# Optimization experiments

Hardware: AMD Instinct MI355X
Metric: run time of the kernel (lower is better)

The kernel has to match this reference:

```python
import jax, jax.numpy as jnp
import numpy as np

N_HEAD = 32


def _apply_rope(x, rope):
    # x: (B, H, T, hs); rope: (block_size, hs//2) angles
    B, H, T, hs = x.shape
    ang = rope[:T]  # (T, hs//2)
    cos = jnp.cos(ang)[None, :, None, :]  # (1, T, 1, hs//2)
    sin = jnp.sin(ang)[None, :, None, :]
    xt = x.transpose(0, 2, 1, 3).reshape(B, T, H, hs // 2, 2)
    x0, x1 = xt[..., 0], xt[..., 1]
    out_r = x0 * cos - x1 * sin
    out_i = x0 * sin + x1 * cos
    out = jnp.stack([out_r, out_i], axis=-1).reshape(B, T, H, hs)
    return out.transpose(0, 2, 1, 3)


def setup_inputs() -> dict:
    key = jax.random.key(0)
    ks = jax.random.split(key, 6)
    B, T, C = 2, 2048, 4096
    aT = 10
    hs = C // N_HEAD
    return {
        "x": jax.random.normal(ks[0], (B, T, C), dtype=jnp.float32),
        "adaption_prompt": jax.random.normal(ks[1], (1, aT, C), dtype=jnp.float32),
        "rope_cache": jax.random.uniform(ks[2], (4096, hs // 2), dtype=jnp.float32) * 2.0 * np.pi,
        "w_attn": jax.random.normal(ks[3], (C, 3 * C), dtype=jnp.float32) * 0.02,
        "w_proj": jax.random.normal(ks[4], (C, C), dtype=jnp.float32) * 0.02,
        "gating_factor": jax.random.normal(ks[5], (1,), dtype=jnp.float32) * 0.1,
    }


def reference(x, adaption_prompt, rope_cache, w_attn, w_proj, gating_factor):
    B, T, C = x.shape
    H = N_HEAD
    hs = C // H

    qkv = x @ w_attn  # (B, T, 3C)
    q, k, v = jnp.split(qkv, 3, axis=2)
    q = q.reshape(B, T, H, hs).transpose(0, 2, 1, 3)  # (B, H, T, hs)
    k = k.reshape(B, T, H, hs).transpose(0, 2, 1, 3)
    v = v.reshape(B, T, H, hs).transpose(0, 2, 1, 3)

    q = _apply_rope(q, rope_cache)
    k = _apply_rope(k, rope_cache)

    # causal SDPA, scale = 1/sqrt(head_size)
    scale = 1.0 / jnp.sqrt(jnp.asarray(hs, dtype=q.dtype))
    scores = jnp.einsum("bhqd,bhkd->bhqk", q, k) * scale
    causal = jnp.tril(jnp.ones((T, T), dtype=bool))
    scores = jnp.where(causal[None, None, :, :], scores, jnp.asarray(-jnp.inf, scores.dtype))
    attn = jax.nn.softmax(scores, axis=-1)
    y = jnp.einsum("bhqk,bhkd->bhqd", attn, v)  # (B, H, T, hs)

    # adapter attention (note: scale uses full n_embd, as in source)
    aT = adaption_prompt.shape[1]
    aqkv = adaption_prompt @ w_attn  # (1, aT, 3C)
    _, ak, av = jnp.split(aqkv, 3, axis=2)
    ak = ak.reshape(1, aT, H, hs).transpose(0, 2, 1, 3)  # (1, H, aT, hs)
    av = av.reshape(1, aT, H, hs).transpose(0, 2, 1, 3)
    ascores = jnp.einsum("bhqd,xhkd->bhqk", q, ak) / jnp.sqrt(jnp.asarray(C, q.dtype))
    ascores = gating_factor[0] * jax.nn.softmax(ascores.astype(jnp.float32), axis=-1).astype(q.dtype)
    y = y + jnp.einsum("bhqk,xhkd->bhqd", ascores, av)

    y = y.transpose(0, 2, 1, 3).reshape(B, T, C)
    return y @ w_proj
```

## Files before the change

kernel.cpp:

```cpp
#include <hip/hip_runtime.h>

typedef unsigned short u16;
typedef unsigned int u32;
typedef __attribute__((ext_vector_type(4))) float f32x4;
typedef __attribute__((ext_vector_type(8))) _Float16 half8;
typedef __attribute__((ext_vector_type(8))) unsigned short u16x8;
typedef __attribute__((ext_vector_type(4))) unsigned short u16x4;

static __device__ __forceinline__ u16 f2h(float f) {
  union { _Float16 h; u16 u; } c;
  c.h = (_Float16)f;
  return c.u;
}
static __device__ __forceinline__ float h2f(u16 u) {
  union { _Float16 h; u16 u; } c;
  c.u = u;
  return (float)c.h;
}
static __device__ __forceinline__ void gload_lds16(const void* g, void* l) {
  __builtin_amdgcn_global_load_lds((const __attribute__((address_space(1))) void*)g,
                                   (__attribute__((address_space(3))) void*)l,
                                   16, 0, 0);
}

__global__ __launch_bounds__(256) void transpose_cvt(const float* __restrict__ src,
                                                     u16* __restrict__ dst,
                                                     int R, int C) {
  __shared__ float tile[32][33];
  const int tx = threadIdx.x, ty = threadIdx.y;
  const int c0 = blockIdx.x << 5, r0 = blockIdx.y << 5;
#pragma unroll
  for (int i = 0; i < 32; i += 8)
    tile[ty + i][tx] = src[(size_t)(r0 + ty + i) * C + c0 + tx];
  __syncthreads();
#pragma unroll
  for (int i = 0; i < 32; i += 8)
    dst[(size_t)(c0 + ty + i) * R + r0 + tx] = f2h(tile[tx][ty + i]);
}

__global__ __launch_bounds__(256) void cvt_f32_f16(const float* __restrict__ in,
                                                   u16* __restrict__ out, int n4) {
  int i = blockIdx.x * 256 + threadIdx.x;
  if (i >= n4) return;
  f32x4 v = *(const f32x4*)(in + (size_t)i * 4);
  u16x4 o;
  o[0] = f2h(v[0]); o[1] = f2h(v[1]); o[2] = f2h(v[2]); o[3] = f2h(v[3]);
  *(u16x4*)(out + (size_t)i * 4) = o;
}

static __device__ __forceinline__ void store_out(float* C, size_t idx, float v) { C[idx] = v; }
static __device__ __forceinline__ void store_out(u16* C, size_t idx, float v) { C[idx] = f2h(v); }

static __device__ __forceinline__ void stageA(const u16* __restrict__ Ab, int K, int kt,
                                              u16* As, int mh, int t) {
#pragma unroll
  for (int i = 0; i < 2; ++i) {
    int row = i * 128 + mh * 64 + (t >> 3);
    int slot = t & 7;
    gload_lds16(Ab + (size_t)row * K + kt + ((slot ^ (row & 7)) << 3),
                (char*)As + (size_t)(i * 128 + mh * 64) * 128 + t * 16);
  }
}
static __device__ __forceinline__ void stageB(const u16* __restrict__ Bb, int K, int kt,
                                              u16* Bs, int nh, int t) {
#pragma unroll
  for (int i = 0; i < 2; ++i) {
    int j = (t >> 8) + 2 * i;
    int rem = t & 255;
    int row = j * 64 + nh * 32 + (rem >> 3);
    int slot = rem & 7;
    gload_lds16(Bb + (size_t)row * K + kt + ((slot ^ (row & 7)) << 3),
                (char*)Bs + (size_t)(j * 64 + nh * 32) * 128 + rem * 16);
  }
}

#define DO_PHASE(AS, BS, MH, NH, STAGE_STMT, WAIT_STR)                           \
  {                                                                              \
    half8 af[4][2], bf[2][2];                                                    \
    _Pragma("unroll") for (int mf = 0; mf < 4; ++mf)                             \
      _Pragma("unroll") for (int kk = 0; kk < 2; ++kk) {                         \
        int row = wm * 128 + ((MH) * 4 + mf) * 16 + l15;                         \
        int slot = (kk * 4 + g) ^ (l15 & 7);                                     \
        af[mf][kk] = *(const half8*)((const char*)(AS) + row * 128 + slot * 16); \
      }                                                                          \
    _Pragma("unroll") for (int nf = 0; nf < 2; ++nf)                             \
      _Pragma("unroll") for (int kk = 0; kk < 2; ++kk) {                         \
        int row = wn * 64 + ((NH) * 2 + nf) * 16 + l15;                          \
        int slot = (kk * 4 + g) ^ (l15 & 7);                                     \
        bf[nf][kk] = *(const half8*)((const char*)(BS) + row * 128 + slot * 16); \
      }                                                                          \
    STAGE_STMT;                                                                  \
    asm volatile("s_barrier" ::: "memory");                                      \
    __builtin_amdgcn_s_setprio(1);                                               \
    _Pragma("unroll") for (int kk = 0; kk < 2; ++kk)                             \
      _Pragma("unroll") for (int mf = 0; mf < 4; ++mf)                           \
        _Pragma("unroll") for (int nf = 0; nf < 2; ++nf)                         \
          acc[(MH) * 4 + mf][(NH) * 2 + nf] =                                    \
              __builtin_amdgcn_mfma_f32_16x16x32_f16(                            \
                  af[mf][kk], bf[nf][kk], acc[(MH) * 4 + mf][(NH) * 2 + nf],     \
                  0, 0, 0);                                                      \
    __builtin_amdgcn_s_setprio(0);                                               \
    asm volatile(WAIT_STR ::: "memory");                                         \
  }

template <typename OutT>
__global__ __launch_bounds__(512, 2) void gemm256(const u16* __restrict__ A,
                                                  const u16* __restrict__ Bt,
                                                  OutT* __restrict__ C,
                                                  int M, int N, int K, int nbn) {
  __shared__ u16 lds[4][16384];
  const int t = threadIdx.x;
  const int lane = t & 63;
  const int wid = t >> 6;
  const int g = lane >> 4, l15 = lane & 15;
  const int wm = wid >> 2, wn = wid & 3;
  const int nwg = gridDim.x;
  const int bid = blockIdx.x;
  const int wgid = (bid & 7) * (nwg >> 3) + (bid >> 3);
  const int bm = wgid / nbn, bn = wgid % nbn;
  const u16* Ab = A + (size_t)bm * 256 * K;
  const u16* Bb = Bt + (size_t)bn * 256 * K;
  f32x4 acc[8][4] = {};

  stageB(Bb, K, 0, lds[1], 0, t);
  stageA(Ab, K, 0, lds[0], 0, t);
  stageB(Bb, K, 0, lds[1], 1, t);
  stageA(Ab, K, 0, lds[0], 1, t);
  stageB(Bb, K, 64, lds[3], 0, t);
  stageA(Ab, K, 64, lds[2], 0, t);
  asm volatile("s_waitcnt vmcnt(4)\ns_barrier" ::: "memory");

  const int nit = K >> 7;
  for (int i = 0; i < nit; ++i) {
    int k1 = (2 * i + 1) << 6;
    int k2 = (2 * i + 2) << 6; if (k2 >= K) k2 = 0;
    int k3 = (2 * i + 3) << 6; if (k3 >= K) k3 = 0;
    DO_PHASE(lds[0], lds[1], 0, 0, stageB(Bb, K, k1, lds[3], 1, t), "s_waitcnt vmcnt(6)\ns_barrier");
    DO_PHASE(lds[0], lds[1], 1, 0, stageA(Ab, K, k1, lds[2], 1, t), "s_barrier");
    DO_PHASE(lds[0], lds[1], 0, 1, stageB(Bb, K, k2, lds[1], 0, t), "s_barrier");
    DO_PHASE(lds[0], lds[1], 1, 1, stageA(Ab, K, k2, lds[0], 0, t), "s_waitcnt vmcnt(8)\ns_barrier");
    DO_PHASE(lds[2], lds[3], 0, 0, stageB(Bb, K, k2, lds[1], 1, t), "s_waitcnt vmcnt(6)\ns_barrier");
    DO_PHASE(lds[2], lds[3], 1, 0, stageA(Ab, K, k2, lds[0], 1, t), "s_barrier");
    DO_PHASE(lds[2], lds[3], 0, 1, stageB(Bb, K, k3, lds[3], 0, t), "s_barrier");
    DO_PHASE(lds[2], lds[3], 1, 1, stageA(Ab, K, k3, lds[2], 0, t), "s_waitcnt vmcnt(8)\ns_barrier");
  }
  asm volatile("s_waitcnt vmcnt(0)" ::: "memory");

#pragma unroll
  for (int mf = 0; mf < 8; ++mf) {
    int row0 = bm * 256 + wm * 128 + mf * 16 + 4 * g;
#pragma unroll
    for (int nf = 0; nf < 4; ++nf) {
      int col = bn * 256 + wn * 64 + nf * 16 + l15;
#pragma unroll
      for (int r = 0; r < 4; ++r)
        store_out(C, (size_t)(row0 + r) * N + col, acc[mf][nf][r]);
    }
  }
}

__global__ __launch_bounds__(256) void rope_kernel(u16* __restrict__ qkv,
                                                   const float* __restrict__ rope) {
  int idx = blockIdx.x * 256 + threadIdx.x;
  int bt = idx >> 12;
  int pp = idx & 4095;
  int part = pp >> 11;
  int within = pp & 2047;
  int hh = within >> 6;
  int p = within & 63;
  int tpos = bt & 2047;
  size_t off = (size_t)bt * 12288 + part * 4096 + hh * 128 + 2 * p;
  u32* ptr = (u32*)(qkv + off);
  u32 v = *ptr;
  float x0 = h2f((u16)(v & 0xffff));
  float x1 = h2f((u16)(v >> 16));
  float sn, cs;
  __sincosf(rope[tpos * 64 + p], &sn, &cs);
  float y0 = x0 * cs - x1 * sn;
  float y1 = x0 * sn + x1 * cs;
  *ptr = (u32)f2h(y0) | ((u32)f2h(y1) << 16);
}

__global__ __launch_bounds__(256) void v_transpose(const u16* __restrict__ qkv,
                                                   u16* __restrict__ vt) {
  __shared__ u16 tile[64 * 128];
  const int bx = blockIdx.x;
  const int tt = bx & 31, h = (bx >> 5) & 31, b = bx >> 10;
  const u16* src = qkv + (size_t)b * 2048 * 12288 + 8192 + h * 128;
  const int t = threadIdx.x;
#pragma unroll
  for (int i = 0; i < 4; ++i) {
    int c = t + 256 * i;
    int row = c >> 4, slot = c & 15;
    u16x8 v = *(const u16x8*)(src + (size_t)(tt * 64 + row) * 12288 + slot * 8);
    *(u16x8*)(tile + row * 128 + ((slot ^ (row >> 3)) << 3)) = v;
  }
  __syncthreads();
  u16* dst = vt + (size_t)(b * 32 + h) * 128 * 2048 + tt * 64;
#pragma unroll
  for (int i = 0; i < 4; ++i) {
    int c = t + 256 * i;
    int drow = c >> 3, t8 = c & 7;
    u16x8 o;
#pragma unroll
    for (int e = 0; e < 8; ++e) {
      int row = t8 * 8 + e;
      int slot = (drow >> 3) ^ (row >> 3);
      o[e] = tile[row * 128 + (slot << 3) + (drow & 7)];
    }
    *(u16x8*)(dst + (size_t)drow * 2048 + t8 * 8) = o;
  }
}

__global__ __launch_bounds__(256) void adaption_kv_kernel(const float* __restrict__ prompt,
                                                          const float* __restrict__ w_attn,
                                                          u16* __restrict__ akbuf,
                                                          u16* __restrict__ avbuf) {
  __shared__ float pl[10][512];
  __shared__ float red[8][10][32];
  const int t = threadIdx.x;
  const int tc = t & 31, tk = t >> 5;
  const int n = blockIdx.x * 32 + tc;
  float acc[10] = {};
  for (int k0 = 0; k0 < 4096; k0 += 512) {
    __syncthreads();
#pragma unroll
    for (int i = 0; i < 20; ++i) {
      int idx = t + 256 * i;
      int j = idx >> 9, kk = idx & 511;
      pl[j][kk] = prompt[(size_t)j * 4096 + k0 + kk];
    }
    __syncthreads();
    for (int kk = tk; kk < 512; kk += 8) {
      float wv = w_attn[(size_t)(k0 + kk) * 12288 + 4096 + n];
#pragma unroll
      for (int j = 0; j < 10; ++j) acc[j] += pl[j][kk] * wv;
    }
  }
  __syncthreads();
#pragma unroll
  for (int j = 0; j < 10; ++j) red[tk][j][tc] = acc[j];
  __syncthreads();
  if (tk == 0) {
    float s[10];
#pragma unroll
    for (int j = 0; j < 10; ++j) {
      s[j] = 0.f;
#pragma unroll
      for (int q = 0; q < 8; ++q) s[j] += red[q][j][tc];
    }
    u16* dst;
    int hh, d;
    if (n < 4096) { dst = akbuf; hh = n >> 7; d = n & 127; }
    else          { dst = avbuf; hh = (n - 4096) >> 7; d = n & 127; }
#pragma unroll
    for (int j = 0; j < 16; ++j)
      dst[(size_t)(hh * 16 + j) * 128 + d] = (j < 10) ? f2h(s[j]) : (u16)0;
  }
}

__global__ __launch_bounds__(256) void attn_kernel(const u16* __restrict__ qkv,
                                                   const u16* __restrict__ vt,
                                                   const u16* __restrict__ akbuf,
                                                   const u16* __restrict__ avbuf,
                                                   const float* __restrict__ gating,
                                                   u16* __restrict__ y) {
  __shared__ u16 Kl[64 * 128];
  __shared__ u16 Vtl[128 * 64];
  __shared__ u16 Pl[4][16 * 64];

  const int t = threadIdx.x;
  const int lane = t & 63, w = t >> 6;
  const int g = lane >> 4, l15 = lane & 15;
  const int bx = blockIdx.x;
  const int qb = 31 - (bx >> 6);
  const int bh = bx & 63, b = bh >> 5, h = bh & 31;
  const int ldq = 12288;
  const u16* Qg = qkv + (size_t)b * 2048 * ldq + h * 128;
  const u16* Kg = Qg + 4096;
  const u16* VtG = vt + (size_t)(b * 32 + h) * 128 * 2048;
  u16* AKb = &Pl[0][0];

#pragma unroll
  for (int i = 0; i < 4; ++i) {
    int c = t + 256 * i;
    int row = c >> 4, slot = c & 15;
    gload_lds16(Qg + (size_t)(qb * 64 + row) * ldq + ((slot ^ (row & 15)) << 3),
                (char*)Kl + c * 16);
  }
  {
    int row = t >> 4, slot = t & 15;
    gload_lds16(akbuf + (size_t)(h * 16 + row) * 128 + ((slot ^ row) << 3),
                (char*)AKb + t * 16);
  }
  __syncthreads();

  half8 qf[4];
#pragma unroll
  for (int kk = 0; kk < 4; ++kk) {
    int slot = (kk * 4 + g) ^ l15;
    qf[kk] = *(const half8*)((const char*)Kl + (w * 16 + l15) * 256 + (slot << 4));
  }
  f32x4 sa = {};
#pragma unroll
  for (int kk = 0; kk < 4; ++kk) {
    int slot = (kk * 4 + g) ^ l15;
    half8 af = *(const half8*)((const char*)AKb + l15 * 256 + (slot << 4));
    sa = __builtin_amdgcn_mfma_f32_16x16x32_f16(qf[kk], af, sa, 0, 0, 0);
  }
  __syncthreads();

  f32x4 acc[8] = {};
  float mrun[4], lrun[4];
#pragma unroll
  for (int r = 0; r < 4; ++r) { mrun[r] = -1e30f; lrun[r] = 0.f; }

  for (int kvt = 0; kvt <= qb; ++kvt) {
#pragma unroll
    for (int i = 0; i < 4; ++i) {
      int c = t + 256 * i;
      int row = c >> 4, slot = c & 15;
      gload_lds16(Kg + (size_t)(kvt * 64 + row) * ldq + ((slot ^ (row & 15)) << 3),
                  (char*)Kl + c * 16);
    }
#pragma unroll
    for (int i = 0; i < 4; ++i) {
      int c = t + 256 * i;
      int d = c >> 3, s3 = c & 7;
      gload_lds16(VtG + (size_t)d * 2048 + kvt * 64 + ((s3 ^ (d & 7)) << 3),
                  (char*)Vtl + c * 16);
    }
    __syncthreads();

    f32x4 s[4] = {};
#pragma unroll
    for (int nf = 0; nf < 4; ++nf) {
#pragma unroll
      for (int kk = 0; kk < 4; ++kk) {
        int slot = (kk * 4 + g) ^ l15;
        half8 kf = *(const half8*)((const char*)Kl + (nf * 16 + l15) * 256 + (slot << 4));
        s[nf] = __builtin_amdgcn_mfma_f32_16x16x32_f16(qf[kk], kf, s[nf], 0, 0, 0);
      }
    }
    const float sc = 0.08838834764831843f;
    if (kvt == qb) {
#pragma unroll
      for (int nf = 0; nf < 4; ++nf)
#pragma unroll
        for (int r = 0; r < 4; ++r) {
          int kv = nf * 16 + l15;
          int qq = w * 16 + 4 * g + r;
          float v = s[nf][r] * sc;
          s[nf][r] = (kv <= qq) ? v : -1e30f;
        }
    } else {
#pragma unroll
      for (int nf = 0; nf < 4; ++nf)
#pragma unroll
        for (int r = 0; r < 4; ++r) s[nf][r] *= sc;
    }

    float alpha[4];
#pragma unroll
    for (int r = 0; r < 4; ++r) {
      float mt = fmaxf(fmaxf(s[0][r], s[1][r]), fmaxf(s[2][r], s[3][r]));
#pragma unroll
      for (int off = 1; off < 16; off <<= 1)
        mt = fmaxf(mt, __shfl_xor(mt, off, 64));
      float mn = fmaxf(mrun[r], mt);
      alpha[r] = __expf(mrun[r] - mn);
      mrun[r] = mn;
      float rs = 0.f;
#pragma unroll
      for (int nf = 0; nf < 4; ++nf) {
        float p = __expf(s[nf][r] - mn);
        s[nf][r] = p;
        rs += p;
      }
#pragma unroll
      for (int off = 1; off < 16; off <<= 1)
        rs += __shfl_xor(rs, off, 64);
      lrun[r] = lrun[r] * alpha[r] + rs;
    }
#pragma unroll
    for (int nd = 0; nd < 8; ++nd)
#pragma unroll
      for (int r = 0; r < 4; ++r)
        acc[nd][r] *= alpha[r];

#pragma unroll
    for (int nf = 0; nf < 4; ++nf)
#pragma unroll
      for (int r = 0; r < 4; ++r) {
        int qq = 4 * g + r;
        int kv = nf * 16 + l15;
        int byteoff = (qq * 128 + kv * 2) ^ ((qq & 7) << 4);
        *(u16*)((char*)Pl[w] + byteoff) = f2h(s[nf][r]);
      }

#pragma unroll
    for (int kk2 = 0; kk2 < 2; ++kk2) {
      int pslot = (kk2 * 4 + g) ^ (l15 & 7);
      half8 pf = *(const half8*)((const char*)Pl[w] + l15 * 128 + (pslot << 4));
#pragma unroll
      for (int nd = 0; nd < 8; ++nd) {
        int d = nd * 16 + l15;
        int slot = (kk2 * 4 + g) ^ (d & 7);
        half8 vf = *(const half8*)((const char*)Vtl + d * 128 + (slot << 4));
        acc[nd] = __builtin_amdgcn_mfma_f32_16x16x32_f16(pf, vf, acc[nd], 0, 0, 0);
      }
    }
    __syncthreads();
  }

  {
    int d = t >> 1;
    int jb = (t & 1) << 4;
#pragma unroll
    for (int i = 0; i < 16; ++i) {
      int j = jb + i;
      u16 v = (j < 16) ? avbuf[(size_t)(h * 16 + j) * 128 + d] : (u16)0;
      int byteoff = (d * 64 + j * 2) ^ ((d & 3) << 4);
      *(u16*)((char*)Kl + byteoff) = v;
    }
  }
  __syncthreads();

  float ga = gating[0];
  float pa4[4];
#pragma unroll
  for (int r = 0; r < 4; ++r) {
    float v = sa[r] * (1.0f / 64.0f);
    if (l15 >= 10) v = -1e30f;
    float mt = v;
#pragma unroll
    for (int off = 1; off < 16; off <<= 1)
      mt = fmaxf(mt, __shfl_xor(mt, off, 64));
    float p = __expf(v - mt);
    float rs = p;
#pragma unroll
    for (int off = 1; off < 16; off <<= 1)
      rs += __shfl_xor(rs, off, 64);
    pa4[r] = p / rs * ga;
  }
#pragma unroll
  for (int r = 0; r < 4; ++r) {
    float inv = 1.0f / lrun[r];
#pragma unroll
    for (int nd = 0; nd < 8; ++nd)
      acc[nd][r] *= inv;
  }
#pragma unroll
  for (int r = 0; r < 4; ++r) {
    int qq = 4 * g + r;
    int b1 = (qq * 128 + l15 * 2) ^ ((qq & 7) << 4);
    *(u16*)((char*)Pl[w] + b1) = f2h(pa4[r]);
    int b2 = (qq * 128 + (16 + l15) * 2) ^ ((qq & 7) << 4);
    *(u16*)((char*)Pl[w] + b2) = 0;
  }
  {
    int pslot = g ^ (l15 & 7);
    half8 pf = *(const half8*)((const char*)Pl[w] + l15 * 128 + (pslot << 4));
#pragma unroll
    for (int nd = 0; nd < 8; ++nd) {
      int d = nd * 16 + l15;
      int byteoff = (d * 64 + g * 16) ^ ((d & 3) << 4);
      half8 avf = *(const half8*)((const char*)Kl + byteoff);
      acc[nd] = __builtin_amdgcn_mfma_f32_16x16x32_f16(pf, avf, acc[nd], 0, 0, 0);
    }
  }
#pragma unroll
  for (int nd = 0; nd < 8; ++nd) {
    int col = h * 128 + nd * 16 + l15;
#pragma unroll
    for (int r = 0; r < 4; ++r) {
      int row = qb * 64 + w * 16 + 4 * g + r;
      y[(size_t)(b * 2048 + row) * 4096 + col] = f2h(acc[nd][r]);
    }
  }
}

extern "C" void kernel_launch(void* const* d_in, const int* in_sizes, int n_in,
                              void* d_out, int out_size, void* d_ws, size_t ws_size,
                              hipStream_t stream) {
  (void)in_sizes; (void)n_in; (void)out_size; (void)ws_size;
  const float* x      = (const float*)d_in[0];
  const float* prompt = (const float*)d_in[1];
  const float* rope   = (const float*)d_in[2];
  const float* w_attn = (const float*)d_in[3];
  const float* w_proj = (const float*)d_in[4];
  const float* gating = (const float*)d_in[5];
  float* out = (float*)d_out;

  char* ws = (char*)d_ws;
  u16* WtA = (u16*)(ws);
  u16* Yb  = (u16*)(ws);
  u16* VtG = (u16*)(ws + 33554432);
  u16* qkv = (u16*)(ws + 100663296);
  u16* xb  = (u16*)(ws + 201326592);
  u16* WtP = (u16*)(ws + 201326592);
  u16* akb = (u16*)(ws + 234881024);
  u16* avb = (u16*)(ws + 234881024 + 131072);

  transpose_cvt<<<dim3(384, 128), dim3(32, 8), 0, stream>>>(w_attn, WtA, 4096, 12288);
  cvt_f32_f16<<<dim3(16384), dim3(256), 0, stream>>>(x, xb, 4194304);
  gemm256<u16><<<dim3(768), dim3(512), 0, stream>>>(xb, WtA, qkv, 4096, 12288, 4096, 48);
  rope_kernel<<<dim3(65536), dim3(256), 0, stream>>>(qkv, rope);
  v_transpose<<<dim3(2048), dim3(256), 0, stream>>>(qkv, VtG);
  adaption_kv_kernel<<<dim3(256), dim3(256), 0, stream>>>(prompt, w_attn, akb, avb);
  attn_kernel<<<dim3(2048), dim3(256), 0, stream>>>(qkv, VtG, akb, avb, gating, Yb);
  transpose_cvt<<<dim3(128, 128), dim3(32, 8), 0, stream>>>(w_proj, WtP, 4096, 4096);
  gemm256<float><<<dim3(256), dim3(512), 0, stream>>>(Yb, WtP, out, 4096, 4096, 4096, 16);
}
```

Measured before the change: 1.049 ms.

## Restructure GEMM main loop into four M-quarter phases with B fragments reused

Reorganizes the 256x256 GEMM pipeline so each K-tile of 64 is processed in four phases over quarters of the A rows. B fragments are loaded from LDS once per tile and reused across all four phases instead of being reloaded per phase. Global-to-LDS staging is split into finer 32-row chunks issued across phases, with new vmcnt wait thresholds. This cuts LDS read traffic for B and changes how loads overlap with MFMA. The cost is more live registers for B fragments and a more delicate double-buffer wait schedule that could race or stall if the counts are wrong.

```diff
diff --git a/kernel.cpp b/kernel.cpp
--- a/kernel.cpp
+++ b/kernel.cpp
@@ -53,52 +53,46 @@
 
 static __device__ __forceinline__ void stageA(const u16* __restrict__ Ab, int K, int kt,
                                               u16* As, int mh, int t) {
-#pragma unroll
-  for (int i = 0; i < 2; ++i) {
-    int row = i * 128 + mh * 64 + (t >> 3);
-    int slot = t & 7;
-    gload_lds16(Ab + (size_t)row * K + kt + ((slot ^ (row & 7)) << 3),
-                (char*)As + (size_t)(i * 128 + mh * 64) * 128 + t * 16);
-  }
+  int hf = t >> 8;
+  int tt = t & 255;
+  int row = hf * 128 + mh * 32 + (tt >> 3);
+  int slot = tt & 7;
+  gload_lds16(Ab + (size_t)row * K + kt + ((slot ^ (row & 7)) << 3),
+              (char*)As + hf * 16384 + mh * 4096 + tt * 16);
 }
 static __device__ __forceinline__ void stageB(const u16* __restrict__ Bb, int K, int kt,
-                                              u16* Bs, int nh, int t) {
-#pragma unroll
-  for (int i = 0; i < 2; ++i) {
-    int j = (t >> 8) + 2 * i;
-    int rem = t & 255;
-    int row = j * 64 + nh * 32 + (rem >> 3);
-    int slot = rem & 7;
-    gload_lds16(Bb + (size_t)row * K + kt + ((slot ^ (row & 7)) << 3),
-                (char*)Bs + (size_t)(j * 64 + nh * 32) * 128 + rem * 16);
-  }
-}
-
-#define DO_PHASE(AS, BS, MH, NH, STAGE_STMT, WAIT_STR)                           \
+                                              u16* Bs, int j, int t) {
+  int row = j * 64 + (t >> 3);
+  int slot = t & 7;
+  gload_lds16(Bb + (size_t)row * K + kt + ((slot ^ (row & 7)) << 3),
+              (char*)Bs + j * 8192 + t * 16);
+}
+
+#define LOAD_BF(BS)                                                              \
+  _Pragma("unroll") for (int nf = 0; nf < 4; ++nf)                               \
+    _Pragma("unroll") for (int kk = 0; kk < 2; ++kk) {                           \
+      int row = wn * 64 + nf * 16 + l15;                                         \
+      int slot = (kk * 4 + g) ^ (l15 & 7);                                       \
+      bf[nf][kk] = *(const half8*)((const char*)(BS) + row * 128 + slot * 16);   \
+    }
+
+#define DO_PHASE(AS, Q, STAGE_STMT, WAIT_STR)                                    \
   {                                                                              \
-    half8 af[4][2], bf[2][2];                                                    \
-    _Pragma("unroll") for (int mf = 0; mf < 4; ++mf)                             \
+    half8 af[2][2];                                                              \
+    _Pragma("unroll") for (int mf = 0; mf < 2; ++mf)                             \
       _Pragma("unroll") for (int kk = 0; kk < 2; ++kk) {                         \
-        int row = wm * 128 + ((MH) * 4 + mf) * 16 + l15;                         \
+        int row = wm * 128 + ((Q) * 2 + mf) * 16 + l15;                          \
         int slot = (kk * 4 + g) ^ (l15 & 7);                                     \
         af[mf][kk] = *(const half8*)((const char*)(AS) + row * 128 + slot * 16); \
-      }                                                                          \
-    _Pragma("unroll") for (int nf = 0; nf < 2; ++nf)                             \
-      _Pragma("unroll") for (int kk = 0; kk < 2; ++kk) {                         \
-        int row = wn * 64 + ((NH) * 2 + nf) * 16 + l15;                          \
-        int slot = (kk * 4 + g) ^ (l15 & 7);                                     \
-        bf[nf][kk] = *(const half8*)((const char*)(BS) + row * 128 + slot * 16); \
       }                                                                          \
     STAGE_STMT;                                                                  \
     asm volatile("s_barrier" ::: "memory");                                      \
     __builtin_amdgcn_s_setprio(1);                                               \
     _Pragma("unroll") for (int kk = 0; kk < 2; ++kk)                             \
-      _Pragma("unroll") for (int mf = 0; mf < 4; ++mf)                           \
-        _Pragma("unroll") for (int nf = 0; nf < 2; ++nf)                         \
-          acc[(MH) * 4 + mf][(NH) * 2 + nf] =                                    \
-              __builtin_amdgcn_mfma_f32_16x16x32_f16(                            \
-                  af[mf][kk], bf[nf][kk], acc[(MH) * 4 + mf][(NH) * 2 + nf],     \
-                  0, 0, 0);                                                      \
+      _Pragma("unroll") for (int mf = 0; mf < 2; ++mf)                           \
+        _Pragma("unroll") for (int nf = 0; nf < 4; ++nf)                         \
+          acc[(Q) * 2 + mf][nf] = __builtin_amdgcn_mfma_f32_16x16x32_f16(        \
+              af[mf][kk], bf[nf][kk], acc[(Q) * 2 + mf][nf], 0, 0, 0);           \
     __builtin_amdgcn_s_setprio(0);                                               \
     asm volatile(WAIT_STR ::: "memory");                                         \
   }
@@ -122,27 +116,38 @@
   const u16* Bb = Bt + (size_t)bn * 256 * K;
   f32x4 acc[8][4] = {};
 
+  stageA(Ab, K, 0, lds[0], 0, t);
   stageB(Bb, K, 0, lds[1], 0, t);
-  stageA(Ab, K, 0, lds[0], 0, t);
   stageB(Bb, K, 0, lds[1], 1, t);
+  stageB(Bb, K, 0, lds[1], 2, t);
+  stageB(Bb, K, 0, lds[1], 3, t);
   stageA(Ab, K, 0, lds[0], 1, t);
+  stageA(Ab, K, 0, lds[0], 2, t);
+  stageA(Ab, K, 0, lds[0], 3, t);
   stageB(Bb, K, 64, lds[3], 0, t);
+  stageB(Bb, K, 64, lds[3], 1, t);
   stageA(Ab, K, 64, lds[2], 0, t);
-  asm volatile("s_waitcnt vmcnt(4)\ns_barrier" ::: "memory");
-
-  const int nit = K >> 7;
-  for (int i = 0; i < nit; ++i) {
-    int k1 = (2 * i + 1) << 6;
-    int k2 = (2 * i + 2) << 6; if (k2 >= K) k2 = 0;
-    int k3 = (2 * i + 3) << 6; if (k3 >= K) k3 = 0;
-    DO_PHASE(lds[0], lds[1], 0, 0, stageB(Bb, K, k1, lds[3], 1, t), "s_waitcnt vmcnt(6)\ns_barrier");
-    DO_PHASE(lds[0], lds[1], 1, 0, stageA(Ab, K, k1, lds[2], 1, t), "s_barrier");
-    DO_PHASE(lds[0], lds[1], 0, 1, stageB(Bb, K, k2, lds[1], 0, t), "s_barrier");
-    DO_PHASE(lds[0], lds[1], 1, 1, stageA(Ab, K, k2, lds[0], 0, t), "s_waitcnt vmcnt(8)\ns_barrier");
-    DO_PHASE(lds[2], lds[3], 0, 0, stageB(Bb, K, k2, lds[1], 1, t), "s_waitcnt vmcnt(6)\ns_barrier");
-    DO_PHASE(lds[2], lds[3], 1, 0, stageA(Ab, K, k2, lds[0], 1, t), "s_barrier");
-    DO_PHASE(lds[2], lds[3], 0, 1, stageB(Bb, K, k3, lds[3], 0, t), "s_barrier");
-    DO_PHASE(lds[2], lds[3], 1, 1, stageA(Ab, K, k3, lds[2], 0, t), "s_waitcnt vmcnt(8)\ns_barrier");
+  stageA(Ab, K, 64, lds[2], 1, t);
+  asm volatile("s_waitcnt vmcnt(7)\ns_barrier" ::: "memory");
+
+  const int nt = K >> 6;
+  for (int i = 0; i < nt; ++i) {
+    u16* As = lds[(i & 1) << 1];
+    u16* Bs = lds[((i & 1) << 1) + 1];
+    u16* Asn = lds[((i + 1) & 1) << 1];
+    u16* Bsn = lds[(((i + 1) & 1) << 1) + 1];
+    int k1 = (i + 1) << 6; if (k1 >= K) k1 = 0;
+    int k2 = (i + 2) << 6; if (k2 >= K) k2 = 0;
+    half8 bf[4][2];
+    LOAD_BF(Bs);
+    DO_PHASE(As, 0, { stageB(Bb, K, k1, Bsn, 2, t); stageB(Bb, K, k1, Bsn, 3, t); },
+             "s_waitcnt vmcnt(8)\ns_barrier");
+    DO_PHASE(As, 1, { stageA(Ab, K, k1, Asn, 2, t); stageA(Ab, K, k1, Asn, 3, t); },
+             "s_waitcnt vmcnt(8)\ns_barrier");
+    DO_PHASE(As, 2, { stageB(Bb, K, k2, Bs, 0, t); stageB(Bb, K, k2, Bs, 1, t); },
+             "s_barrier");
+    DO_PHASE(As, 3, { stageA(Ab, K, k2, As, 0, t); stageA(Ab, K, k2, As, 1, t); },
+             "s_waitcnt vmcnt(6)\ns_barrier");
   }
   asm volatile("s_waitcnt vmcnt(0)" ::: "memory");
 
```

After: 1.012 ms. -3.5%, faster.
